# Optimization experiments

Hardware: AMD Instinct MI355X
Metric: run time of the kernel (lower is better)

The kernel has to match this reference:

```python
import jax, jax.numpy as jnp
import numpy as np


def _mdca_one_exit(cam, target):
    # cam: [B, C, H, W] -> adaptive_avg_pool2d(cam, 1).squeeze() == mean over H, W
    logits = cam.mean(axis=(2, 3))            # [B, C]
    B, C = logits.shape
    avg_conf = logits.mean(axis=0)            # [C] per-class mean logit
    counts = jnp.bincount(target, length=C)   # [C] label histogram
    avg_count = counts.astype(logits.dtype) / jnp.asarray(B, logits.dtype)
    return jnp.mean(jnp.abs(avg_conf - avg_count))  # sum/C == mean


def setup_inputs() -> dict:
    key = jax.random.key(0)
    ks = jax.random.split(key, 5)
    B, C, H, W = 128, 1000, 14, 14
    inp = {}
    for i in range(4):
        inp[f'cam_{i}'] = jax.random.normal(ks[i], (B, C, H, W), dtype=jnp.float32)
    inp['target'] = jax.random.randint(ks[4], (B,), 0, C, dtype=jnp.int64)
    return inp


def reference(cam_0, cam_1, cam_2, cam_3, target):
    cams = (cam_0, cam_1, cam_2, cam_3)
    return tuple(_mdca_one_exit(c, target) for c in cams)
```

## Files before the change

kernel.cpp:

```cpp
#include <hip/hip_runtime.h>
#include <hip/hip_bf16.h>


constexpr int B   = 128;
constexpr int C   = 1000;
constexpr int HW  = 196;
constexpr int HW4 = 49;
constexpr int K4  = C * HW4;

__global__ __launch_bounds__(256) void stage1_kernel(
    const float* __restrict__ c0, const float* __restrict__ c1,
    const float* __restrict__ c2, const float* __restrict__ c3,
    float* __restrict__ partial)
{
    const int k   = blockIdx.x * 256 + threadIdx.x;
    const int cam = blockIdx.y;
    const float* __restrict__ src =
        (cam == 0) ? c0 : (cam == 1) ? c1 : (cam == 2) ? c2 : c3;
    if (k >= K4) return;

    const float4* __restrict__ p = reinterpret_cast<const float4*>(src) + k;

    float4 s0 = {0,0,0,0}, s1 = {0,0,0,0}, s2 = {0,0,0,0}, s3 = {0,0,0,0};
    #pragma unroll 2
    for (int b = 0; b < B; b += 4) {
        const float4 v0 = p[(size_t)(b + 0) * K4];
        const float4 v1 = p[(size_t)(b + 1) * K4];
        const float4 v2 = p[(size_t)(b + 2) * K4];
        const float4 v3 = p[(size_t)(b + 3) * K4];
        s0.x += v0.x; s0.y += v0.y; s0.z += v0.z; s0.w += v0.w;
        s1.x += v1.x; s1.y += v1.y; s1.z += v1.z; s1.w += v1.w;
        s2.x += v2.x; s2.y += v2.y; s2.z += v2.z; s2.w += v2.w;
        s3.x += v3.x; s3.y += v3.y; s3.z += v3.z; s3.w += v3.w;
    }
    const float t0 = (s0.x + s0.y) + (s0.z + s0.w);
    const float t1 = (s1.x + s1.y) + (s1.z + s1.w);
    const float t2 = (s2.x + s2.y) + (s2.z + s2.w);
    const float t3 = (s3.x + s3.y) + (s3.z + s3.w);
    partial[cam * K4 + k] = (t0 + t1) + (t2 + t3);
}

__global__ __launch_bounds__(1024) void stage2_kernel(
    const float* __restrict__ partial, const int* __restrict__ target,
    float* __restrict__ out)
{
    __shared__ int   cnt[C];
    __shared__ float red[16];

    const int cam = blockIdx.x;
    const int tid = threadIdx.x;

    for (int i = tid; i < C; i += 1024) cnt[i] = 0;
    __syncthreads();
    if (tid < B) atomicAdd(&cnt[target[tid]], 1);
    __syncthreads();

    float acc = 0.0f;
    if (tid < C) {
        const float* __restrict__ q = partial + cam * K4 + tid * HW4;
        float ssum = 0.0f;
        #pragma unroll 7
        for (int j = 0; j < HW4; ++j) ssum += q[j];
        acc = fabsf(ssum * (1.0f / (float)(B * HW))
                    - (float)cnt[tid] * (1.0f / (float)B));
    }

    #pragma unroll
    for (int off = 32; off > 0; off >>= 1)
        acc += __shfl_down(acc, off, 64);
    if ((tid & 63) == 0) red[tid >> 6] = acc;
    __syncthreads();
    if (tid == 0) {
        float s = 0.0f;
        #pragma unroll
        for (int w = 0; w < 16; ++w) s += red[w];
        out[cam] = s * (1.0f / (float)C);
    }
}

extern "C" void kernel_launch(void* const* d_in, const int* in_sizes, int n_in,
                              void* d_out, int out_size, void* d_ws, size_t ws_size,
                              hipStream_t stream) {
    const float* c0 = (const float*)d_in[0];
    const float* c1 = (const float*)d_in[1];
    const float* c2 = (const float*)d_in[2];
    const float* c3 = (const float*)d_in[3];
    const int*   target = (const int*)d_in[4];

    float* partial = (float*)d_ws;

    dim3 grid1((K4 + 255) / 256, 4);
    stage1_kernel<<<grid1, 256, 0, stream>>>(c0, c1, c2, c3, partial);
    stage2_kernel<<<4, 1024, 0, stream>>>(partial, target, (float*)d_out);
}
```

Baseline: 82.28 us.

## Reduce contiguous HW segments per wavefront with scan-based segmented sums

Stage 1 now streams each cam fully contiguously. Each wavefront reads 64 consecutive float4 per iteration and uses a wave-wide prefix scan plus readlane to split the values into per-(b,c) spatial sums. The old scheme read with a batch stride of about 196KB. Stage 2 then sums across batch per class from the new [B,C] segment sums. This trades strided access for extra shuffle and scan ALU work per float4, and adds a fallback path that runs two passes when the workspace is small.

```diff
diff --git a/kernel.cpp b/kernel.cpp
--- a/kernel.cpp
+++ b/kernel.cpp
@@ -2,79 +2,97 @@
 #include <hip/hip_bf16.h>
 
 
-constexpr int B   = 128;
-constexpr int C   = 1000;
-constexpr int HW  = 196;
-constexpr int HW4 = 49;
-constexpr int K4  = C * HW4;
+constexpr int B    = 128;
+constexpr int C    = 1000;
+constexpr int HW   = 196;
+constexpr int HW4  = 49;
+constexpr int NSEG = B * C;
+constexpr int NF4  = NSEG * HW4;
+constexpr int RUN4 = 64 * HW4;
+constexpr int NRUN = NF4 / RUN4;
+
+__device__ __forceinline__ float lane_read(float v, int src) {
+    return __int_as_float(__builtin_amdgcn_readlane(__float_as_int(v), src));
+}
 
 __global__ __launch_bounds__(256) void stage1_kernel(
     const float* __restrict__ c0, const float* __restrict__ c1,
     const float* __restrict__ c2, const float* __restrict__ c3,
-    float* __restrict__ partial)
+    float* __restrict__ segsum, int cam_base)
 {
-    const int k   = blockIdx.x * 256 + threadIdx.x;
-    const int cam = blockIdx.y;
+    const int lane = threadIdx.x & 63;
+    const int run  = blockIdx.x * 4 + (threadIdx.x >> 6);
+    const int cam  = cam_base + blockIdx.y;
     const float* __restrict__ src =
         (cam == 0) ? c0 : (cam == 1) ? c1 : (cam == 2) ? c2 : c3;
-    if (k >= K4) return;
 
-    const float4* __restrict__ p = reinterpret_cast<const float4*>(src) + k;
+    const float4* __restrict__ p =
+        reinterpret_cast<const float4*>(src) + (size_t)run * RUN4 + lane;
 
-    float4 s0 = {0,0,0,0}, s1 = {0,0,0,0}, s2 = {0,0,0,0}, s3 = {0,0,0,0};
-    #pragma unroll 2
-    for (int b = 0; b < B; b += 4) {
-        const float4 v0 = p[(size_t)(b + 0) * K4];
-        const float4 v1 = p[(size_t)(b + 1) * K4];
-        const float4 v2 = p[(size_t)(b + 2) * K4];
-        const float4 v3 = p[(size_t)(b + 3) * K4];
-        s0.x += v0.x; s0.y += v0.y; s0.z += v0.z; s0.w += v0.w;
-        s1.x += v1.x; s1.y += v1.y; s1.z += v1.z; s1.w += v1.w;
-        s2.x += v2.x; s2.y += v2.y; s2.z += v2.z; s2.w += v2.w;
-        s3.x += v3.x; s3.y += v3.y; s3.z += v3.z; s3.w += v3.w;
+    float acc = 0.0f;
+    #pragma unroll 7
+    for (int i = 0; i < 49; ++i) {
+        const float4 v = p[i * 64];
+        float sc = (v.x + v.y) + (v.z + v.w);
+
+        #pragma unroll
+        for (int off = 1; off < 64; off <<= 1) {
+            const float y = __shfl_up(sc, off, 64);
+            if (lane >= off) sc += y;
+        }
+
+        const int r  = (15 * i) % 49;
+        const int l1 = 49 - r;
+        const int g0 = (64 * i) / 49;
+        const int bx = (l1 + 48 > 63) ? 63 : (l1 + 48);
+
+        const float SA = lane_read(sc, l1 - 1);
+        const float SB = lane_read(sc, bx);
+        const float ST = lane_read(sc, 63);
+
+        if (lane == g0)     acc += SA;
+        if (lane == g0 + 1) acc += SB - SA;
+        if (lane == g0 + 2) acc += ST - SB;
     }
-    const float t0 = (s0.x + s0.y) + (s0.z + s0.w);
-    const float t1 = (s1.x + s1.y) + (s1.z + s1.w);
-    const float t2 = (s2.x + s2.y) + (s2.z + s2.w);
-    const float t3 = (s3.x + s3.y) + (s3.z + s3.w);
-    partial[cam * K4 + k] = (t0 + t1) + (t2 + t3);
+
+    segsum[(size_t)blockIdx.y * NSEG + (size_t)run * 64 + lane] = acc;
 }
 
 __global__ __launch_bounds__(1024) void stage2_kernel(
-    const float* __restrict__ partial, const int* __restrict__ target,
-    float* __restrict__ out)
+    const float* __restrict__ segsum, const int* __restrict__ target,
+    float* __restrict__ out, int cam_base)
 {
     __shared__ int   cnt[C];
     __shared__ float red[16];
 
-    const int cam = blockIdx.x;
-    const int tid = threadIdx.x;
+    const int slot = blockIdx.x;
+    const int tid  = threadIdx.x;
 
     for (int i = tid; i < C; i += 1024) cnt[i] = 0;
     __syncthreads();
     if (tid < B) atomicAdd(&cnt[target[tid]], 1);
     __syncthreads();
 
-    float acc = 0.0f;
+    float a = 0.0f;
     if (tid < C) {
-        const float* __restrict__ q = partial + cam * K4 + tid * HW4;
-        float ssum = 0.0f;
-        #pragma unroll 7
-        for (int j = 0; j < HW4; ++j) ssum += q[j];
-        acc = fabsf(ssum * (1.0f / (float)(B * HW))
-                    - (float)cnt[tid] * (1.0f / (float)B));
+        const float* __restrict__ q = segsum + (size_t)slot * NSEG + tid;
+        float t = 0.0f;
+        #pragma unroll 8
+        for (int b = 0; b < B; ++b) t += q[b * 1000];
+        a = fabsf(t * (1.0f / (float)(B * HW))
+                  - (float)cnt[tid] * (1.0f / (float)B));
     }
 
     #pragma unroll
     for (int off = 32; off > 0; off >>= 1)
-        acc += __shfl_down(acc, off, 64);
-    if ((tid & 63) == 0) red[tid >> 6] = acc;
+        a += __shfl_down(a, off, 64);
+    if ((tid & 63) == 0) red[tid >> 6] = a;
     __syncthreads();
     if (tid == 0) {
         float s = 0.0f;
         #pragma unroll
         for (int w = 0; w < 16; ++w) s += red[w];
-        out[cam] = s * (1.0f / (float)C);
+        out[cam_base + slot] = s * (1.0f / (float)C);
     }
 }
 
@@ -86,10 +104,20 @@
     const float* c2 = (const float*)d_in[2];
     const float* c3 = (const float*)d_in[3];
     const int*   target = (const int*)d_in[4];
+    float*       out    = (float*)d_out;
+    float*       segsum = (float*)d_ws;
 
-    float* partial = (float*)d_ws;
+    const size_t need4 = (size_t)4 * NSEG * sizeof(float);
 
-    dim3 grid1((K4 + 255) / 256, 4);
-    stage1_kernel<<<grid1, 256, 0, stream>>>(c0, c1, c2, c3, partial);
-    stage2_kernel<<<4, 1024, 0, stream>>>(partial, target, (float*)d_out);
+    if (ws_size >= need4) {
+        dim3 g1(NRUN / 4, 4);
+        stage1_kernel<<<g1, 256, 0, stream>>>(c0, c1, c2, c3, segsum, 0);
+        stage2_kernel<<<4, 1024, 0, stream>>>(segsum, target, out, 0);
+    } else {
+        dim3 g1(NRUN / 4, 2);
+        stage1_kernel<<<g1, 256, 0, stream>>>(c0, c1, c2, c3, segsum, 0);
+        stage2_kernel<<<2, 1024, 0, stream>>>(segsum, target, out, 0);
+        stage1_kernel<<<g1, 256, 0, stream>>>(c0, c1, c2, c3, segsum, 2);
+        stage2_kernel<<<2, 1024, 0, stream>>>(segsum, target, out, 2);
+    }
 }
```

After: 86.24 us. 4.8% more time.
